# Optimization experiments

Measured on AMD Instinct MI355X. Metric: run time of the kernel, lower is better.

## Reference

```python
import jax, jax.numpy as jnp
import numpy as np

H = 16      # num heads
DH = 64     # head dim
D = H * DH  # hidden = 1024

def setup_inputs() -> dict:
    key = jax.random.key(0)
    ks = jax.random.split(key, 8)
    B, S = 4, 2048
    scale = 1.0 / np.sqrt(D)
    return {
        "hidden_states": jax.random.normal(ks[0], (B, S, D), dtype=jnp.float32),
        "attention_mask": jnp.zeros((B, S, S), dtype=jnp.float32),
        "Wq": jax.random.normal(ks[1], (D, D), dtype=jnp.float32) * scale,
        "bq": jnp.zeros((D,), dtype=jnp.float32),
        "Wk": jax.random.normal(ks[2], (D, D), dtype=jnp.float32) * scale,
        "bk": jnp.zeros((D,), dtype=jnp.float32),
        "Wv": jax.random.normal(ks[3], (D, D), dtype=jnp.float32) * scale,
        "bv": jnp.zeros((D,), dtype=jnp.float32),
    }

def _split_heads(x):
    B, S, _ = x.shape
    return x.reshape(B, S, H, DH).transpose(0, 2, 1, 3)  # [B,H,S,dh]

def reference(hidden_states, attention_mask, Wq, bq, Wk, bk, Wv, bv):
    q = _split_heads(hidden_states @ Wq + bq)
    k = _split_heads(hidden_states @ Wk + bk)
    v = _split_heads(hidden_states @ Wv + bv)
    scores = jnp.einsum("bhqd,bhkd->bhqk", q, k) / jnp.sqrt(jnp.float32(DH))
    scores = scores + attention_mask[:, None, :, :]
    probs = jax.nn.softmax(scores, axis=-1)  # dropout p=0 (eval) -> identity
    ctx = jnp.einsum("bhqk,bhkd->bhqd", probs, v)
    B, _, S, _ = ctx.shape
    return ctx.transpose(0, 2, 1, 3).reshape(B, S, H * DH)
```

## Files before the change

### kernel.cpp

```cpp
#include <hip/hip_runtime.h>

typedef __bf16 bf16;
typedef __bf16 bf16x8 __attribute__((ext_vector_type(8)));
typedef __bf16 bf16x4 __attribute__((ext_vector_type(4)));
typedef float floatx4 __attribute__((ext_vector_type(4)));

typedef __attribute__((address_space(1))) void gvoid;
typedef __attribute__((address_space(3))) void lvoid;
#define ASYNC_COPY16(gp, lp) \
  __builtin_amdgcn_global_load_lds((gvoid*)(gp), (lvoid*)(lp), 16, 0, 0)

#define NB 4
#define SQ 2048
#define DMODEL 1024
#define NH 16
#define HD 64
#define MTOK (NB * SQ)

#define XB_OFF 0ull
#define WT_OFF (16ull * 1024 * 1024)
#define Q_OFF  (22ull * 1024 * 1024)
#define K_OFF  (38ull * 1024 * 1024)
#define V_OFF  (54ull * 1024 * 1024)
#define FLG_OFF (70ull * 1024 * 1024)

__global__ void convert_x(const float* __restrict__ x, bf16* __restrict__ xb) {
  int i = blockIdx.x * blockDim.x + threadIdx.x;
  float4 v = ((const float4*)x)[i];
  bf16x4 o;
  o[0] = (bf16)v.x; o[1] = (bf16)v.y; o[2] = (bf16)v.z; o[3] = (bf16)v.w;
  ((bf16x4*)xb)[i] = o;
}

__global__ void transpose_w(const float* __restrict__ w0,
                            const float* __restrict__ w1,
                            const float* __restrict__ w2,
                            bf16* __restrict__ wt) {
  __shared__ float t[32][33];
  const float* w = (blockIdx.z == 0) ? w0 : (blockIdx.z == 1) ? w1 : w2;
  bf16* out = wt + (size_t)blockIdx.z * DMODEL * DMODEL;
  int kb = blockIdx.y * 32, nb = blockIdx.x * 32;
  int tx = threadIdx.x, ty = threadIdx.y;
#pragma unroll
  for (int i = 0; i < 4; i++)
    t[ty + 8 * i][tx] = w[(size_t)(kb + ty + 8 * i) * DMODEL + nb + tx];
  __syncthreads();
#pragma unroll
  for (int i = 0; i < 4; i++)
    out[(size_t)(nb + ty + 8 * i) * DMODEL + kb + tx] = (bf16)t[tx][ty + 8 * i];
}

__global__ void mask_scan(const float* __restrict__ mask, int* __restrict__ flags) {
  int b = blockIdx.z, qt = blockIdx.y, kt = blockIdx.x;
  const float* mb = mask + ((size_t)b * SQ + qt * 128) * SQ + kt * 64;
  int t = threadIdx.x;
  int row = t >> 1, half = t & 1;
  const float4* p = (const float4*)(mb + (size_t)row * SQ + half * 32);
  bool nz = false;
#pragma unroll
  for (int i = 0; i < 8; i++) {
    float4 v = p[i];
    nz |= (v.x != 0.f) | (v.y != 0.f) | (v.z != 0.f) | (v.w != 0.f);
  }
  __shared__ int acc;
  if (t == 0) acc = 0;
  __syncthreads();
  unsigned long long m = __ballot(nz);
  if ((t & 63) == 0 && m) atomicOr(&acc, 1);
  __syncthreads();
  if (t == 0) flags[(b * 16 + qt) * 32 + kt] = acc;
}

#define BK 64
__global__ __launch_bounds__(256) void qkv_gemm(
    const bf16* __restrict__ xb,
    const bf16* __restrict__ wt,
    const float* __restrict__ biasq, const float* __restrict__ biask,
    const float* __restrict__ biasv,
    bf16* __restrict__ q, bf16* __restrict__ k, bf16* __restrict__ v) {
  __shared__ bf16 As[128 * BK];
  __shared__ bf16 Bs[128 * BK];

  int mt = blockIdx.x;
  int nt = blockIdx.y;
  int mat = nt >> 3;
  int nbase = (nt & 7) * 128;
  const bf16* wmat = wt + (size_t)mat * DMODEL * DMODEL;
  const float* bias = (mat == 0) ? biasq : (mat == 1) ? biask : biasv;
  bf16* outp = (mat == 0) ? q : (mat == 1) ? k : v;

  int t = threadIdx.x;
  int lane = t & 63, wid = t >> 6;
  int quad = lane >> 4, l16 = lane & 15;
  int wm = (wid & 1) * 64, wn = (wid >> 1) * 64;

  floatx4 acc[4][4] = {};

  for (int kb = 0; kb < DMODEL; kb += BK) {
    __syncthreads();
#pragma unroll
    for (int p = 0; p < 4; p++) {
      int idx = p * 256 + t;
      int row = idx >> 3;
      int ch = idx & 7;
      ASYNC_COPY16(xb + (size_t)(mt * 128 + row) * DMODEL + kb + ch * 8,
                   As + idx * 8);
      ASYNC_COPY16(wmat + (size_t)(nbase + row) * DMODEL + kb + ch * 8,
                   Bs + idx * 8);
    }
    __syncthreads();

#pragma unroll
    for (int kc = 0; kc < BK; kc += 32) {
      bf16x8 af[4], bfr[4];
#pragma unroll
      for (int mi = 0; mi < 4; mi++)
        af[mi] = *(const bf16x8*)(As + (wm + mi * 16 + l16) * BK + kc + quad * 8);
#pragma unroll
      for (int ni = 0; ni < 4; ni++)
        bfr[ni] = *(const bf16x8*)(Bs + (wn + ni * 16 + l16) * BK + kc + quad * 8);
#pragma unroll
      for (int mi = 0; mi < 4; mi++)
#pragma unroll
        for (int ni = 0; ni < 4; ni++)
          acc[mi][ni] = __builtin_amdgcn_mfma_f32_16x16x32_bf16(
              af[mi], bfr[ni], acc[mi][ni], 0, 0, 0);
    }
  }

  int mg0 = mt * 128 + wm;
#pragma unroll
  for (int ni = 0; ni < 4; ni++) {
    int n = nbase + wn + ni * 16 + l16;
    int h = n >> 6, d = n & 63;
    float bv_ = bias[n];
    if (mat < 2) {
#pragma unroll
      for (int mi = 0; mi < 4; mi++) {
#pragma unroll
        for (int r = 0; r < 4; r++) {
          int m = mg0 + mi * 16 + quad * 4 + r;
          int b = m >> 11, s = m & 2047;
          float val = acc[mi][ni][r] + bv_;
          if (mat == 0) val *= 0.125f;
          outp[(((size_t)(b * NH + h) * SQ + s) << 6) + d] = (bf16)val;
        }
      }
    } else {
#pragma unroll
      for (int mi = 0; mi < 4; mi++) {
        int m0 = mg0 + mi * 16 + quad * 4;
        int b = m0 >> 11, s = m0 & 2047;
        bf16x4 pk;
#pragma unroll
        for (int r = 0; r < 4; r++) pk[r] = (bf16)(acc[mi][ni][r] + bv_);
        *(bf16x4*)(outp + (((size_t)(b * NH + h) * HD + d) << 11) + s) = pk;
      }
    }
  }
}

#define PPAD 72
__global__ __launch_bounds__(256, 4) void attn(
    const bf16* __restrict__ Q,
    const bf16* __restrict__ K,
    const bf16* __restrict__ Vt,
    const float* __restrict__ mask,
    const int* __restrict__ flags,
    float* __restrict__ out) {
  __shared__ bf16 Ks[64 * 64];
  __shared__ bf16 Vs[64 * 64];
  __shared__ bf16 P[4][32][PPAD];

  int bh = blockIdx.x;
  int qt = blockIdx.y;
  int b = bh >> 4, h = bh & 15;
  int t = threadIdx.x, lane = t & 63, wid = t >> 6;
  int quad = lane >> 4, l16 = lane & 15;
  int q0 = qt * 128 + wid * 32;

  const bf16* Qp = Q + ((size_t)bh * SQ + q0) * HD;
  const bf16* Kp = K + (size_t)bh * SQ * HD;
  const bf16* Vp = Vt + (size_t)bh * HD * SQ;
  const float* mp = mask + ((size_t)b * SQ + q0) * SQ;
  const int* flg = flags + (b * 16 + qt) * 32;

  bf16x8 qa[2][2];
#pragma unroll
  for (int m = 0; m < 2; m++) {
    const bf16* qr = Qp + (size_t)(m * 16 + l16) * HD;
    qa[m][0] = *(const bf16x8*)(qr + quad * 8);
    qa[m][1] = *(const bf16x8*)(qr + 32 + quad * 8);
  }

  floatx4 o[2][4] = {};
  float li[2] = {0.f, 0.f};
  bf16* Pw = &P[wid][0][0];
  int xq = quad ^ (l16 & 7);

  for (int kb = 0, kti = 0; kb < SQ; kb += 64, kti++) {
    __syncthreads();
#pragma unroll
    for (int p = 0; p < 2; p++) {
      int idx = p * 256 + t;
      int row = idx >> 3;
      int gch = (idx ^ row) & 7;
      ASYNC_COPY16(Kp + (size_t)(kb + row) * HD + gch * 8, Ks + idx * 8);
      ASYNC_COPY16(Vp + (size_t)row * SQ + kb + gch * 8, Vs + idx * 8);
    }
    __syncthreads();
    int flag = flg[kti];

    float xs[2][4][4];
#pragma unroll
    for (int kt = 0; kt < 4; kt++) {
      const bf16* kr = Ks + (kt * 16 + l16) * 64;
      bf16x8 k0 = *(const bf16x8*)(kr + xq * 8);
      bf16x8 k1 = *(const bf16x8*)(kr + (xq ^ 4) * 8);
      floatx4 z0 = {}, z1 = {};
      z0 = __builtin_amdgcn_mfma_f32_16x16x32_bf16(k0, qa[0][0], z0, 0, 0, 0);
      z0 = __builtin_amdgcn_mfma_f32_16x16x32_bf16(k1, qa[0][1], z0, 0, 0, 0);
      z1 = __builtin_amdgcn_mfma_f32_16x16x32_bf16(k0, qa[1][0], z1, 0, 0, 0);
      z1 = __builtin_amdgcn_mfma_f32_16x16x32_bf16(k1, qa[1][1], z1, 0, 0, 0);
#pragma unroll
      for (int r = 0; r < 4; r++) { xs[0][kt][r] = z0[r]; xs[1][kt][r] = z1[r]; }
    }
    if (flag) {
#pragma unroll
      for (int m = 0; m < 2; m++)
#pragma unroll
        for (int kt = 0; kt < 4; kt++)
#pragma unroll
          for (int r = 0; r < 4; r++)
            xs[m][kt][r] += mp[(size_t)(m * 16 + l16) * SQ + kb + kt * 16 + quad * 4 + r];
    }

#pragma unroll
    for (int m = 0; m < 2; m++) {
      float sum = 0.f;
#pragma unroll
      for (int kt = 0; kt < 4; kt++) {
        bf16x4 pk;
#pragma unroll
        for (int r = 0; r < 4; r++) {
          float e = __expf(xs[m][kt][r]);
          sum += e;
          pk[r] = (bf16)e;
        }
        *(bf16x4*)(Pw + (m * 16 + l16) * PPAD + kt * 16 + quad * 4) = pk;
      }
      li[m] += sum;
    }
    asm volatile("s_waitcnt lgkmcnt(0)" ::: "memory");
    bf16x8 pb[2][2];
#pragma unroll
    for (int m = 0; m < 2; m++) {
      pb[m][0] = *(const bf16x8*)(Pw + (m * 16 + l16) * PPAD + quad * 8);
      pb[m][1] = *(const bf16x8*)(Pw + (m * 16 + l16) * PPAD + 32 + quad * 8);
    }

#pragma unroll
    for (int dt = 0; dt < 4; dt++) {
      const bf16* vr = Vs + (dt * 16 + l16) * 64;
      bf16x8 v0 = *(const bf16x8*)(vr + xq * 8);
      bf16x8 v1 = *(const bf16x8*)(vr + (xq ^ 4) * 8);
      o[0][dt] = __builtin_amdgcn_mfma_f32_16x16x32_bf16(v0, pb[0][0], o[0][dt], 0, 0, 0);
      o[0][dt] = __builtin_amdgcn_mfma_f32_16x16x32_bf16(v1, pb[0][1], o[0][dt], 0, 0, 0);
      o[1][dt] = __builtin_amdgcn_mfma_f32_16x16x32_bf16(v0, pb[1][0], o[1][dt], 0, 0, 0);
      o[1][dt] = __builtin_amdgcn_mfma_f32_16x16x32_bf16(v1, pb[1][1], o[1][dt], 0, 0, 0);
    }
  }
#pragma unroll
  for (int m = 0; m < 2; m++) {
    li[m] += __shfl_xor(li[m], 16, 64);
    li[m] += __shfl_xor(li[m], 32, 64);
  }
#pragma unroll
  for (int m = 0; m < 2; m++) {
    float inv = 1.0f / li[m];
    float* op = out + ((size_t)b * SQ + q0 + m * 16 + l16) * DMODEL + h * HD;
#pragma unroll
    for (int dt = 0; dt < 4; dt++)
#pragma unroll
      for (int r = 0; r < 4; r++)
        op[dt * 16 + quad * 4 + r] = o[m][dt][r] * inv;
  }
}

extern "C" void kernel_launch(void* const* d_in, const int* in_sizes, int n_in,
                              void* d_out, int out_size, void* d_ws, size_t ws_size,
                              hipStream_t stream) {
  (void)in_sizes; (void)n_in; (void)out_size; (void)ws_size;
  const float* hs   = (const float*)d_in[0];
  const float* mask = (const float*)d_in[1];
  const float* Wq   = (const float*)d_in[2];
  const float* bq   = (const float*)d_in[3];
  const float* Wk   = (const float*)d_in[4];
  const float* bk   = (const float*)d_in[5];
  const float* Wv   = (const float*)d_in[6];
  const float* bv   = (const float*)d_in[7];
  float* out = (float*)d_out;
  char* ws = (char*)d_ws;
  bf16* xb = (bf16*)(ws + XB_OFF);
  bf16* wt = (bf16*)(ws + WT_OFF);
  bf16* q  = (bf16*)(ws + Q_OFF);
  bf16* k  = (bf16*)(ws + K_OFF);
  bf16* v  = (bf16*)(ws + V_OFF);
  int* flg = (int*)(ws + FLG_OFF);

  convert_x<<<MTOK * DMODEL / 4 / 256, 256, 0, stream>>>(hs, xb);
  transpose_w<<<dim3(32, 32, 3), dim3(32, 8), 0, stream>>>(Wq, Wk, Wv, wt);
  mask_scan<<<dim3(32, 16, 4), 256, 0, stream>>>(mask, flg);
  qkv_gemm<<<dim3(64, 24), 256, 0, stream>>>(xb, wt, bq, bk, bv, q, k, v);
  attn<<<dim3(64, 16), 256, 0, stream>>>(q, k, v, mask, flg, out);
}
```

Baseline: 318.1 us.

## Merge prep kernels, fuse mask scan into QKV GEMM launch, use exp2

```diff
diff --git a/kernel.cpp b/kernel.cpp
--- a/kernel.cpp
+++ b/kernel.cpp
@@ -16,6 +16,7 @@
 #define NH 16
 #define HD 64
 #define MTOK (NB * SQ)
+#define LOG2E 1.44269504088896f
 
 #define XB_OFF 0ull
 #define WT_OFF (16ull * 1024 * 1024)
@@ -24,72 +25,83 @@
 #define V_OFF  (54ull * 1024 * 1024)
 #define FLG_OFF (70ull * 1024 * 1024)
 
-__global__ void convert_x(const float* __restrict__ x, bf16* __restrict__ xb) {
-  int i = blockIdx.x * blockDim.x + threadIdx.x;
-  float4 v = ((const float4*)x)[i];
-  bf16x4 o;
-  o[0] = (bf16)v.x; o[1] = (bf16)v.y; o[2] = (bf16)v.z; o[3] = (bf16)v.w;
-  ((bf16x4*)xb)[i] = o;
+__global__ __launch_bounds__(256) void prep(
+    const float* __restrict__ x, bf16* __restrict__ xb,
+    const float* __restrict__ w0, const float* __restrict__ w1,
+    const float* __restrict__ w2, bf16* __restrict__ wt) {
+  __shared__ float tlds[32][33];
+  int blk = blockIdx.x;
+  int t = threadIdx.x;
+  if (blk < 8192) {
+    int i = blk * 256 + t;
+    float4 v = ((const float4*)x)[i];
+    bf16x4 o;
+    o[0] = (bf16)v.x; o[1] = (bf16)v.y; o[2] = (bf16)v.z; o[3] = (bf16)v.w;
+    ((bf16x4*)xb)[i] = o;
+  } else {
+    int tidx = blk - 8192;
+    int z = tidx >> 10;
+    int rem = tidx & 1023;
+    int kb = ((rem >> 5) & 31) * 32, nb = (rem & 31) * 32;
+    const float* w = (z == 0) ? w0 : (z == 1) ? w1 : w2;
+    bf16* out = wt + (size_t)z * DMODEL * DMODEL;
+    int tx = t & 31, ty = t >> 5;
+#pragma unroll
+    for (int i = 0; i < 4; i++)
+      tlds[ty + 8 * i][tx] = w[(size_t)(kb + ty + 8 * i) * DMODEL + nb + tx];
+    __syncthreads();
+#pragma unroll
+    for (int i = 0; i < 4; i++)
+      out[(size_t)(nb + ty + 8 * i) * DMODEL + kb + tx] = (bf16)tlds[tx][ty + 8 * i];
+  }
 }
 
-__global__ void transpose_w(const float* __restrict__ w0,
-                            const float* __restrict__ w1,
-                            const float* __restrict__ w2,
-                            bf16* __restrict__ wt) {
-  __shared__ float t[32][33];
-  const float* w = (blockIdx.z == 0) ? w0 : (blockIdx.z == 1) ? w1 : w2;
-  bf16* out = wt + (size_t)blockIdx.z * DMODEL * DMODEL;
-  int kb = blockIdx.y * 32, nb = blockIdx.x * 32;
-  int tx = threadIdx.x, ty = threadIdx.y;
-#pragma unroll
-  for (int i = 0; i < 4; i++)
-    t[ty + 8 * i][tx] = w[(size_t)(kb + ty + 8 * i) * DMODEL + nb + tx];
-  __syncthreads();
-#pragma unroll
-  for (int i = 0; i < 4; i++)
-    out[(size_t)(nb + ty + 8 * i) * DMODEL + kb + tx] = (bf16)t[tx][ty + 8 * i];
-}
-
-__global__ void mask_scan(const float* __restrict__ mask, int* __restrict__ flags) {
-  int b = blockIdx.z, qt = blockIdx.y, kt = blockIdx.x;
-  const float* mb = mask + ((size_t)b * SQ + qt * 128) * SQ + kt * 64;
-  int t = threadIdx.x;
-  int row = t >> 1, half = t & 1;
-  const float4* p = (const float4*)(mb + (size_t)row * SQ + half * 32);
-  bool nz = false;
-#pragma unroll
-  for (int i = 0; i < 8; i++) {
-    float4 v = p[i];
-    nz |= (v.x != 0.f) | (v.y != 0.f) | (v.z != 0.f) | (v.w != 0.f);
-  }
-  __shared__ int acc;
-  if (t == 0) acc = 0;
-  __syncthreads();
-  unsigned long long m = __ballot(nz);
-  if ((t & 63) == 0 && m) atomicOr(&acc, 1);
-  __syncthreads();
-  if (t == 0) flags[(b * 16 + qt) * 32 + kt] = acc;
-}
-
 #define BK 64
-__global__ __launch_bounds__(256) void qkv_gemm(
+__global__ __launch_bounds__(256) void qkv_mask(
     const bf16* __restrict__ xb,
     const bf16* __restrict__ wt,
     const float* __restrict__ biasq, const float* __restrict__ biask,
     const float* __restrict__ biasv,
-    bf16* __restrict__ q, bf16* __restrict__ k, bf16* __restrict__ v) {
+    bf16* __restrict__ q, bf16* __restrict__ k, bf16* __restrict__ v,
+    const float* __restrict__ mask, int* __restrict__ flags) {
   __shared__ bf16 As[128 * BK];
   __shared__ bf16 Bs[128 * BK];
 
-  int mt = blockIdx.x;
-  int nt = blockIdx.y;
+  int idx = blockIdx.x;
+  int r7 = idx % 7, d7 = idx / 7;
+  int t = threadIdx.x;
+
+  if (r7 >= 3) {
+    int midx = d7 * 4 + (r7 - 3);
+    int kt = midx & 31, qt = (midx >> 5) & 15, b = midx >> 9;
+    const float* mb = mask + ((size_t)b * SQ + qt * 128) * SQ + kt * 64;
+    int row = t >> 1, half = t & 1;
+    const float4* p = (const float4*)(mb + (size_t)row * SQ + half * 32);
+    bool nz = false;
+#pragma unroll
+    for (int i = 0; i < 8; i++) {
+      float4 vv = p[i];
+      nz |= (vv.x != 0.f) | (vv.y != 0.f) | (vv.z != 0.f) | (vv.w != 0.f);
+    }
+    int* acc = (int*)As;
+    if (t == 0) acc[0] = 0;
+    __syncthreads();
+    unsigned long long m = __ballot(nz);
+    if ((t & 63) == 0 && m) atomicOr(acc, 1);
+    __syncthreads();
+    if (t == 0) flags[(b * 16 + qt) * 32 + kt] = acc[0];
+    return;
+  }
+
+  int qidx = d7 * 3 + r7;
+  int mt = qidx & 63;
+  int nt = qidx >> 6;
   int mat = nt >> 3;
   int nbase = (nt & 7) * 128;
   const bf16* wmat = wt + (size_t)mat * DMODEL * DMODEL;
   const float* bias = (mat == 0) ? biasq : (mat == 1) ? biask : biasv;
   bf16* outp = (mat == 0) ? q : (mat == 1) ? k : v;
 
-  int t = threadIdx.x;
   int lane = t & 63, wid = t >> 6;
   int quad = lane >> 4, l16 = lane & 15;
   int wm = (wid & 1) * 64, wn = (wid >> 1) * 64;
@@ -100,13 +112,13 @@
     __syncthreads();
 #pragma unroll
     for (int p = 0; p < 4; p++) {
-      int idx = p * 256 + t;
-      int row = idx >> 3;
-      int ch = idx & 7;
+      int i2 = p * 256 + t;
+      int row = i2 >> 3;
+      int ch = i2 & 7;
       ASYNC_COPY16(xb + (size_t)(mt * 128 + row) * DMODEL + kb + ch * 8,
-                   As + idx * 8);
+                   As + i2 * 8);
       ASYNC_COPY16(wmat + (size_t)(nbase + row) * DMODEL + kb + ch * 8,
-                   Bs + idx * 8);
+                   Bs + i2 * 8);
     }
     __syncthreads();
 
@@ -142,7 +154,7 @@
           int m = mg0 + mi * 16 + quad * 4 + r;
           int b = m >> 11, s = m & 2047;
           float val = acc[mi][ni][r] + bv_;
-          if (mat == 0) val *= 0.125f;
+          if (mat == 0) val *= 0.125f * LOG2E;
           outp[(((size_t)(b * NH + h) * SQ + s) << 6) + d] = (bf16)val;
         }
       }
@@ -232,7 +244,9 @@
         for (int kt = 0; kt < 4; kt++)
 #pragma unroll
           for (int r = 0; r < 4; r++)
-            xs[m][kt][r] += mp[(size_t)(m * 16 + l16) * SQ + kb + kt * 16 + quad * 4 + r];
+            xs[m][kt][r] = __builtin_fmaf(
+                mp[(size_t)(m * 16 + l16) * SQ + kb + kt * 16 + quad * 4 + r],
+                LOG2E, xs[m][kt][r]);
     }
 
 #pragma unroll
@@ -243,7 +257,7 @@
         bf16x4 pk;
 #pragma unroll
         for (int r = 0; r < 4; r++) {
-          float e = __expf(xs[m][kt][r]);
+          float e = __builtin_amdgcn_exp2f(xs[m][kt][r]);
           sum += e;
           pk[r] = (bf16)e;
         }
@@ -308,9 +322,7 @@
   bf16* v  = (bf16*)(ws + V_OFF);
   int* flg = (int*)(ws + FLG_OFF);
 
-  convert_x<<<MTOK * DMODEL / 4 / 256, 256, 0, stream>>>(hs, xb);
-  transpose_w<<<dim3(32, 32, 3), dim3(32, 8), 0, stream>>>(Wq, Wk, Wv, wt);
-  mask_scan<<<dim3(32, 16, 4), 256, 0, stream>>>(mask, flg);
-  qkv_gemm<<<dim3(64, 24), 256, 0, stream>>>(xb, wt, bq, bk, bv, q, k, v);
+  prep<<<8192 + 3072, 256, 0, stream>>>(hs, xb, Wq, Wk, Wv, wt);
+  qkv_mask<<<3584, 256, 0, stream>>>(xb, wt, bq, bk, bv, q, k, v, mask, flg);
   attn<<<dim3(64, 16), 256, 0, stream>>>(q, k, v, mask, flg, out);
 }
```

Result: no change. 317.1 us (-0.3%).
